# Kernel tuning notes

Hardware: AMD Instinct MI355X
Metric: run time of the kernel (lower is better)

## Reference

```python
import jax, jax.numpy as jnp
import numpy as np
from jax.ops import segment_sum

N = 100000   # nodes
E = 1600000  # edges
D = 128      # node_feature_dim == hidden_dim
DE = 16      # edge_feature_dim
G = 512      # num_graphs
EPS = 1e-5   # BatchNorm eps


def setup_inputs() -> dict:
    key = jax.random.key(0)
    ks = jax.random.split(key, 24)
    inp = {
        "x": jax.random.normal(ks[0], (N, D), jnp.float32),
        "edge_index": jax.random.randint(ks[1], (2, E), 0, N, jnp.int64),
        "batch_idx": jnp.sort(jax.random.randint(ks[2], (N,), 0, G, jnp.int64)),
        "edge_attr": jax.random.normal(ks[3], (E, DE), jnp.float32),
        "num_graphs": G,
    }
    s = 1.0 / np.sqrt(D)
    # GCN layer 1 (D -> D) + BatchNorm1d (eval-mode running stats)
    inp["W1"] = jax.random.normal(ks[4], (D, D), jnp.float32) * s
    inp["b1"] = jnp.zeros((D,), jnp.float32)
    inp["g1"] = jax.random.uniform(ks[5], (D,), jnp.float32, 0.5, 1.5)
    inp["bt1"] = jax.random.normal(ks[6], (D,), jnp.float32) * 0.1
    inp["m1"] = jax.random.normal(ks[7], (D,), jnp.float32) * 0.1
    inp["v1"] = jax.random.uniform(ks[8], (D,), jnp.float32, 0.5, 1.5)
    # GCN layer 2
    inp["W2"] = jax.random.normal(ks[9], (D, D), jnp.float32) * s
    inp["b2"] = jnp.zeros((D,), jnp.float32)
    inp["g2"] = jax.random.uniform(ks[10], (D,), jnp.float32, 0.5, 1.5)
    inp["bt2"] = jax.random.normal(ks[11], (D,), jnp.float32) * 0.1
    inp["m2"] = jax.random.normal(ks[12], (D,), jnp.float32) * 0.1
    inp["v2"] = jax.random.uniform(ks[13], (D,), jnp.float32, 0.5, 1.5)
    # edge encoder: Linear(DE,D) -> ReLU -> Linear(D,D)
    inp["We1"] = jax.random.normal(ks[14], (DE, D), jnp.float32) / np.sqrt(DE)
    inp["be1"] = jnp.zeros((D,), jnp.float32)
    inp["We2"] = jax.random.normal(ks[15], (D, D), jnp.float32) * s
    inp["be2"] = jnp.zeros((D,), jnp.float32)
    return inp


def _gcn_conv(x, W, b, src, dst, n):
    # PyG GCNConv: add self-loops, sym norm D^-1/2 (A+I) D^-1/2, then X W + b
    xw = x @ W  # [n, out]
    loops = jnp.arange(n, dtype=src.dtype)
    s = jnp.concatenate([src, loops])
    d = jnp.concatenate([dst, loops])
    deg = segment_sum(jnp.ones_like(d, dtype=xw.dtype), d, num_segments=n)
    dinv = jnp.where(deg > 0, jax.lax.rsqrt(jnp.maximum(deg, 1.0)), 0.0)
    norm = dinv[s] * dinv[d]  # [e+n]
    msg = xw[s] * norm[:, None]
    return segment_sum(msg, d, num_segments=n) + b


def _bn_relu(x, g, bt, m, v):
    return jax.nn.relu((x - m) * jax.lax.rsqrt(v + EPS) * g + bt)


def reference(x, edge_index, batch_idx, edge_attr, num_graphs,
              W1, b1, g1, bt1, m1, v1,
              W2, b2, g2, bt2, m2, v2,
              We1, be1, We2, be2):
    n = x.shape[0]
    src, dst = edge_index[0], edge_index[1]
    # two GraphConvLayer: GCNConv -> BN(eval) -> ReLU -> Dropout(eval=id)
    h = _bn_relu(_gcn_conv(x, W1, b1, src, dst, n), g1, bt1, m1, v1)
    h = _bn_relu(_gcn_conv(h, W2, b2, src, dst, n), g2, bt2, m2, v2)
    # global mean pool over nodes per graph
    nsum = segment_sum(h, batch_idx, num_segments=num_graphs)
    ncnt = segment_sum(jnp.ones((n,), h.dtype), batch_idx, num_segments=num_graphs)
    graph_repr = nsum / jnp.maximum(ncnt, 1.0)[:, None]
    # edge encoder + per-graph edge mean (fused segment-mean)
    e = jax.nn.relu(edge_attr @ We1 + be1) @ We2 + be2  # [E, D]
    edge_batch = batch_idx[src]
    esum = segment_sum(e, edge_batch, num_segments=num_graphs)
    ecnt = segment_sum(jnp.ones((e.shape[0],), e.dtype), edge_batch, num_segments=num_graphs)
    edge_repr = jnp.where(ecnt[:, None] > 0, esum / jnp.maximum(ecnt, 1.0)[:, None], 0.0)
    return graph_repr + edge_repr
```

## Files before the change

kernel.cpp:

```cpp
#include <hip/hip_runtime.h>

#define N_NODES 100000
#define N_EDGES 1600000
#define D 128
#define DE 16
#define G 512
#define EPSBN 1e-5f
#define ESLICE 4
#define EPB 1024
#define EPT (EPB / 256)
#define SCHUNK 1024
#define NSB ((N_NODES + SCHUNK - 1) / SCHUNK)
#define AGG_CH 16
#define DSHIFT 9
#define DBSZ 512
#define NBKT ((N_NODES + DBSZ - 1) / DBSZ)

typedef __bf16 bf16x8 __attribute__((ext_vector_type(8)));
typedef __bf16 bf16x4 __attribute__((ext_vector_type(4)));
typedef float f32x4 __attribute__((ext_vector_type(4)));

__device__ __forceinline__ float bf_lo(unsigned v) { return __uint_as_float(v << 16); }
__device__ __forceinline__ float bf_hi(unsigned v) { return __uint_as_float(v & 0xffff0000u); }

__global__ void k_init(int* __restrict__ deg, int* __restrict__ ecnt, int* __restrict__ dcnt,
                       float* __restrict__ gcnt, float* __restrict__ gsum,
                       float* __restrict__ esum) {
  int i = blockIdx.x * 256 + threadIdx.x;
  if (i < N_NODES) deg[i] = 1;
  if (i < G) { ecnt[i] = 0; gcnt[i] = 0.f; }
  if (i < NBKT) dcnt[i] = 0;
  if (i < G * D) { gsum[i] = 0.f; esum[i] = 0.f; }
}

__global__ void k_count(const int* __restrict__ ei, const int* __restrict__ batch,
                        int* __restrict__ deg, int* __restrict__ ecnt, int* __restrict__ dcnt) {
  __shared__ int bins[G];
  __shared__ int dbins[NBKT];
  int tid = threadIdx.x;
  for (int i = tid; i < G; i += 256) bins[i] = 0;
  for (int i = tid; i < NBKT; i += 256) dbins[i] = 0;
  __syncthreads();
  int base = blockIdx.x * 4096;
  for (int t = tid; t < 4096; t += 256) {
    int e = base + t;
    if (e < N_EDGES) {
      int s = ei[e];
      int d = ei[N_EDGES + e];
      atomicAdd(&deg[d], 1);
      atomicAdd(&bins[batch[s]], 1);
      atomicAdd(&dbins[d >> DSHIFT], 1);
    }
  }
  __syncthreads();
  for (int i = tid; i < G; i += 256) if (bins[i]) atomicAdd(&ecnt[i], bins[i]);
  for (int i = tid; i < NBKT; i += 256) if (dbins[i]) atomicAdd(&dcnt[i], dbins[i]);
}

__global__ __launch_bounds__(256) void k_scan_part(const int* __restrict__ deg,
                                                   int* __restrict__ part) {
  __shared__ int red[4];
  int tid = threadIdx.x;
  int base = blockIdx.x * SCHUNK + tid * 4;
  int s = 0;
  #pragma unroll
  for (int k = 0; k < 4; ++k) {
    int i = base + k;
    if (i < N_NODES) s += deg[i];
  }
  #pragma unroll
  for (int off = 32; off > 0; off >>= 1) s += __shfl_down(s, off);
  if ((tid & 63) == 0) red[tid >> 6] = s;
  __syncthreads();
  if (tid == 0) part[blockIdx.x] = red[0] + red[1] + red[2] + red[3];
}

__global__ void k_scan_mid(int* __restrict__ part, const int* __restrict__ ecnt,
                           int* __restrict__ ebs, int* __restrict__ ecur_pad,
                           const int* __restrict__ dcnt, int* __restrict__ dbs,
                           int* __restrict__ dcur_pad) {
  __shared__ int sb[512];
  int tid = threadIdx.x;
  int v = (tid < NSB) ? part[tid] : 0;
  sb[tid] = v;
  __syncthreads();
  for (int off = 1; off < 512; off <<= 1) {
    int t = (tid >= off) ? sb[tid - off] : 0;
    __syncthreads();
    sb[tid] += t;
    __syncthreads();
  }
  if (tid < NSB) part[tid] = sb[tid] - v;
  __syncthreads();
  int v2 = ecnt[tid];
  sb[tid] = v2;
  __syncthreads();
  for (int off = 1; off < 512; off <<= 1) {
    int t = (tid >= off) ? sb[tid - off] : 0;
    __syncthreads();
    sb[tid] += t;
    __syncthreads();
  }
  ebs[tid] = sb[tid] - v2;
  ecur_pad[tid * 16] = sb[tid] - v2;
  __syncthreads();
  int v3 = (tid < NBKT) ? dcnt[tid] : 0;
  sb[tid] = v3;
  __syncthreads();
  for (int off = 1; off < 512; off <<= 1) {
    int t = (tid >= off) ? sb[tid - off] : 0;
    __syncthreads();
    sb[tid] += t;
    __syncthreads();
  }
  if (tid < NBKT) { dbs[tid] = sb[tid] - v3; dcur_pad[tid * 16] = sb[tid] - v3; }
}

__global__ __launch_bounds__(256) void k_scan_write(const int* __restrict__ deg,
                                                    const int* __restrict__ part,
                                                    int* __restrict__ rs,
                                                    float* __restrict__ dinv) {
  __shared__ int sb[256];
  int tid = threadIdx.x;
  int base = blockIdx.x * SCHUNK + tid * 4;
  int d[4];
  int s = 0;
  #pragma unroll
  for (int k = 0; k < 4; ++k) {
    int i = base + k;
    d[k] = (i < N_NODES) ? deg[i] : 0;
    s += d[k];
  }
  sb[tid] = s;
  __syncthreads();
  for (int off = 1; off < 256; off <<= 1) {
    int t = (tid >= off) ? sb[tid - off] : 0;
    __syncthreads();
    sb[tid] += t;
    __syncthreads();
  }
  int ex = sb[tid] - s + part[blockIdx.x];
  #pragma unroll
  for (int k = 0; k < 4; ++k) {
    int i = base + k;
    if (i < N_NODES) {
      rs[i] = ex;
      dinv[i] = rsqrtf((float)d[k]);
      ex += d[k];
    }
  }
}

__global__ __launch_bounds__(256) void k_scatter(const int* __restrict__ ei,
                                                 const int* __restrict__ batch,
                                                 const float* __restrict__ edge_attr,
                                                 int* __restrict__ ecur_pad,
                                                 int* __restrict__ dcur_pad,
                                                 int2* __restrict__ pairs,
                                                 __bf16* __restrict__ eaS) {
  __shared__ int gbins[G];
  __shared__ int gbase[G];
  __shared__ int dbins[NBKT];
  __shared__ int dbase[NBKT];
  int tid = threadIdx.x;
  for (int i = tid; i < G; i += 256) gbins[i] = 0;
  for (int i = tid; i < NBKT; i += 256) dbins[i] = 0;
  __syncthreads();
  int e0 = blockIdx.x * EPB;
  int ge[EPT], gr[EPT], db[EPT], dr[EPT];
  #pragma unroll
  for (int k = 0; k < EPT; ++k) {
    int e = e0 + k * 256 + tid;
    ge[k] = -1;
    if (e < N_EDGES) {
      int s = ei[e], d = ei[N_EDGES + e];
      int g = batch[s];
      ge[k] = g;
      gr[k] = atomicAdd(&gbins[g], 1);
      db[k] = d >> DSHIFT;
      dr[k] = atomicAdd(&dbins[db[k]], 1);
    }
  }
  __syncthreads();
  for (int i = tid; i < G; i += 256) {
    int cnt = gbins[i];
    gbase[i] = cnt ? atomicAdd(&ecur_pad[i * 16], cnt) : 0;
  }
  for (int i = tid; i < NBKT; i += 256) {
    int cnt = dbins[i];
    dbase[i] = cnt ? atomicAdd(&dcur_pad[i * 16], cnt) : 0;
  }
  __syncthreads();
  #pragma unroll
  for (int k = 0; k < EPT; ++k) {
    if (ge[k] >= 0) {
      int e = e0 + k * 256 + tid;
      int s = ei[e], d = ei[N_EDGES + e];
      int gpos = gbase[ge[k]] + gr[k];
      const float4* p = (const float4*)(edge_attr + (size_t)e * DE);
      float4 f0 = p[0], f1 = p[1], f2 = p[2], f3 = p[3];
      bf16x8 h0, h1;
      h0[0] = (__bf16)f0.x; h0[1] = (__bf16)f0.y; h0[2] = (__bf16)f0.z; h0[3] = (__bf16)f0.w;
      h0[4] = (__bf16)f1.x; h0[5] = (__bf16)f1.y; h0[6] = (__bf16)f1.z; h0[7] = (__bf16)f1.w;
      h1[0] = (__bf16)f2.x; h1[1] = (__bf16)f2.y; h1[2] = (__bf16)f2.z; h1[3] = (__bf16)f2.w;
      h1[4] = (__bf16)f3.x; h1[5] = (__bf16)f3.y; h1[6] = (__bf16)f3.z; h1[7] = (__bf16)f3.w;
      bf16x8* q = (bf16x8*)(eaS + (size_t)gpos * DE);
      q[0] = h0; q[1] = h1;
      pairs[dbase[db[k]] + dr[k]] = make_int2(s, d);
    }
  }
}

__global__ __launch_bounds__(256) void k_scatter_nbr(const int2* __restrict__ pairs,
                                                     const int* __restrict__ dbs,
                                                     const int* __restrict__ dcnt,
                                                     const int* __restrict__ rs,
                                                     int* __restrict__ nbr) {
  __shared__ int cur[DBSZ];
  int tid = threadIdx.x;
  int bkt = blockIdx.x;
  int nodeBase = bkt << DSHIFT;
  for (int l = tid; l < DBSZ; l += 256) {
    int node = nodeBase + l;
    cur[l] = (node < N_NODES) ? rs[node] : 0;
  }
  __syncthreads();
  int start = dbs[bkt], n = dcnt[bkt];
  for (int i = tid; i < n; i += 256) {
    int2 p = pairs[start + i];
    int pos = atomicAdd(&cur[p.y - nodeBase], 1);
    nbr[pos] = p.x;
  }
}

__global__ void k_prep_w(const float* __restrict__ W, __bf16* __restrict__ Wf) {
  int tid = threadIdx.x;
  for (int idx = blockIdx.x * 256 + tid; idx < 16384; idx += 8 * 256) {
    int j = idx & 7;
    int lane = (idx >> 3) & 63;
    int cb = (idx >> 9) & 7;
    int kc = idx >> 12;
    int k = kc * 32 + (lane >> 4) * 8 + j;
    int n = cb * 16 + (lane & 15);
    Wf[idx] = (__bf16)W[k * 128 + n];
  }
}

__global__ __launch_bounds__(256) void k_gemm_mfma(const float* __restrict__ X,
                                                   const __bf16* __restrict__ Wf,
                                                   const float* __restrict__ dinv,
                                                   __bf16* __restrict__ out) {
  __shared__ __bf16 sXb[64][136];
  int tid = threadIdx.x;
  int wave = tid >> 6, lane = tid & 63;
  int m = lane & 15, kg = lane >> 4;
  int base = blockIdx.x * 64;
  #pragma unroll
  for (int i = 0; i < 8; ++i) {
    int idx = tid + i * 256;
    int r = idx >> 5, cq = idx & 31;
    int row = base + r;
    float4 v = make_float4(0.f, 0.f, 0.f, 0.f);
    if (row < N_NODES) v = *(const float4*)(X + (size_t)row * 128 + cq * 4);
    bf16x4 h;
    h[0] = (__bf16)v.x; h[1] = (__bf16)v.y; h[2] = (__bf16)v.z; h[3] = (__bf16)v.w;
    *(bf16x4*)(&sXb[r][cq * 4]) = h;
  }
  __syncthreads();
  int r0 = wave * 16;
  f32x4 acc[8];
  #pragma unroll
  for (int cb = 0; cb < 8; ++cb) acc[cb] = (f32x4){0.f, 0.f, 0.f, 0.f};
  #pragma unroll
  for (int kc = 0; kc < 4; ++kc) {
    bf16x8 afrag = *(const bf16x8*)(&sXb[r0 + m][kc * 32 + kg * 8]);
    #pragma unroll
    for (int cb = 0; cb < 8; ++cb) {
      bf16x8 bfrag = *(const bf16x8*)(Wf + (((size_t)(kc * 8 + cb) * 64 + lane) << 3));
      acc[cb] = __builtin_amdgcn_mfma_f32_16x16x32_bf16(afrag, bfrag, acc[cb], 0, 0, 0);
    }
  }
  #pragma unroll
  for (int r = 0; r < 4; ++r) {
    int grow = base + r0 + kg * 4 + r;
    if (grow < N_NODES) {
      float dv = dinv[grow];
      #pragma unroll
      for (int cb = 0; cb < 8; ++cb)
        out[(size_t)grow * 128 + cb * 16 + m] = (__bf16)(acc[cb][r] * dv);
    }
  }
}

__global__ __launch_bounds__(256) void k_agg_bn(const unsigned* __restrict__ Au,
                                                const int* __restrict__ nbr,
                                                const int* __restrict__ rs,
                                                const int* __restrict__ deg,
                                                const float* __restrict__ dinv,
                                                const float* __restrict__ b,
                                                const float* __restrict__ gm,
                                                const float* __restrict__ bt,
                                                const float* __restrict__ m,
                                                const float* __restrict__ v,
                                                float* __restrict__ outB) {
  int tid = threadIdx.x;
  int wave = tid >> 6, lane = tid & 63;
  int c0 = lane * 2, c1 = c0 + 1;
  float sc0 = gm[c0] * rsqrtf(v[c0] + EPSBN), sc1 = gm[c1] * rsqrtf(v[c1] + EPSBN);
  float sh0 = bt[c0] - m[c0] * sc0, sh1 = bt[c1] - m[c1] * sc1;
  float bb0 = b[c0], bb1 = b[c1];
  int base = (blockIdx.x * 4 + wave) * AGG_CH;
  for (int nn = 0; nn < AGG_CH; ++nn) {
    int i = base + nn;
    if (i >= N_NODES) return;
    unsigned sv = Au[(size_t)i * 64 + lane];
    float s0 = bf_lo(sv), s1 = bf_hi(sv);
    int j = rs[i];
    int end = j + deg[i] - 1;
    for (; j + 3 < end; j += 4) {
      int n0 = nbr[j], n1 = nbr[j + 1], n2 = nbr[j + 2], n3 = nbr[j + 3];
      unsigned a0 = Au[(size_t)n0 * 64 + lane];
      unsigned a1 = Au[(size_t)n1 * 64 + lane];
      unsigned a2 = Au[(size_t)n2 * 64 + lane];
      unsigned a3 = Au[(size_t)n3 * 64 + lane];
      s0 += bf_lo(a0) + bf_lo(a1) + bf_lo(a2) + bf_lo(a3);
      s1 += bf_hi(a0) + bf_hi(a1) + bf_hi(a2) + bf_hi(a3);
    }
    for (; j < end; ++j) {
      unsigned a = Au[(size_t)nbr[j] * 64 + lane];
      s0 += bf_lo(a); s1 += bf_hi(a);
    }
    float dv = dinv[i];
    float y0 = fmaxf((dv * s0 + bb0) * sc0 + sh0, 0.f);
    float y1 = fmaxf((dv * s1 + bb1) * sc1 + sh1, 0.f);
    *(float2*)(outB + (size_t)i * 128 + c0) = make_float2(y0, y1);
  }
}

__global__ __launch_bounds__(256) void k_agg_bn_pool(const unsigned* __restrict__ Au,
                                                     const int* __restrict__ nbr,
                                                     const int* __restrict__ rs,
                                                     const int* __restrict__ deg,
                                                     const float* __restrict__ dinv,
                                                     const int* __restrict__ batch,
                                                     const float* __restrict__ b,
                                                     const float* __restrict__ gm,
                                                     const float* __restrict__ bt,
                                                     const float* __restrict__ m,
                                                     const float* __restrict__ v,
                                                     float* __restrict__ gsum,
                                                     float* __restrict__ gcnt) {
  int tid = threadIdx.x;
  int wave = tid >> 6, lane = tid & 63;
  int c0 = lane * 2, c1 = c0 + 1;
  float sc0 = gm[c0] * rsqrtf(v[c0] + EPSBN), sc1 = gm[c1] * rsqrtf(v[c1] + EPSBN);
  float sh0 = bt[c0] - m[c0] * sc0, sh1 = bt[c1] - m[c1] * sc1;
  float bb0 = b[c0], bb1 = b[c1];
  int base = (blockIdx.x * 4 + wave) * AGG_CH;
  if (base >= N_NODES) return;
  float acc0 = 0.f, acc1 = 0.f, cnt = 0.f;
  int curg = -1;
  for (int nn = 0; nn < AGG_CH; ++nn) {
    int i = base + nn;
    if (i >= N_NODES) break;
    int bg = batch[i];
    if (bg != curg) {
      if (curg >= 0) {
        atomicAdd(&gsum[(size_t)curg * 128 + c0], acc0);
        atomicAdd(&gsum[(size_t)curg * 128 + c1], acc1);
        if (lane == 0) atomicAdd(&gcnt[curg], cnt);
      }
      acc0 = 0.f; acc1 = 0.f; cnt = 0.f; curg = bg;
    }
    unsigned sv = Au[(size_t)i * 64 + lane];
    float s0 = bf_lo(sv), s1 = bf_hi(sv);
    int j = rs[i];
    int end = j + deg[i] - 1;
    for (; j + 3 < end; j += 4) {
      int n0 = nbr[j], n1 = nbr[j + 1], n2 = nbr[j + 2], n3 = nbr[j + 3];
      unsigned a0 = Au[(size_t)n0 * 64 + lane];
      unsigned a1 = Au[(size_t)n1 * 64 + lane];
      unsigned a2 = Au[(size_t)n2 * 64 + lane];
      unsigned a3 = Au[(size_t)n3 * 64 + lane];
      s0 += bf_lo(a0) + bf_lo(a1) + bf_lo(a2) + bf_lo(a3);
      s1 += bf_hi(a0) + bf_hi(a1) + bf_hi(a2) + bf_hi(a3);
    }
    for (; j < end; ++j) {
      unsigned a = Au[(size_t)nbr[j] * 64 + lane];
      s0 += bf_lo(a); s1 += bf_hi(a);
    }
    float dv = dinv[i];
    acc0 += fmaxf((dv * s0 + bb0) * sc0 + sh0, 0.f);
    acc1 += fmaxf((dv * s1 + bb1) * sc1 + sh1, 0.f);
    cnt += 1.f;
  }
  if (curg >= 0) {
    atomicAdd(&gsum[(size_t)curg * 128 + c0], acc0);
    atomicAdd(&gsum[(size_t)curg * 128 + c1], acc1);
    if (lane == 0) atomicAdd(&gcnt[curg], cnt);
  }
}

__global__ __launch_bounds__(256) void k_edge_hidden(
    const __bf16* __restrict__ eaS,
    const int* __restrict__ ebs, const int* __restrict__ ecnt,
    const float* __restrict__ We1, const float* __restrict__ be1,
    float* __restrict__ esum) {
  int tid = threadIdx.x;
  int wave = tid >> 6;
  int lane = tid & 63;
  int n = lane & 15;
  int kg = lane >> 4;
  int g = blockIdx.x / ESLICE;
  int slice = blockIdx.x % ESLICE;

  bf16x8 bfrag[8];
  float biasv[8];
  #pragma unroll
  for (int blk = 0; blk < 8; ++blk) {
    #pragma unroll
    for (int j = 0; j < 8; ++j) {
      int k = kg * 8 + j;
      float w = (k < DE) ? We1[k * 128 + blk * 16 + n] : 0.f;
      bfrag[blk][j] = (__bf16)w;
    }
    biasv[blk] = be1[blk * 16 + n];
  }

  int start = ebs[g], cnt = ecnt[g];
  int lim = start + cnt;
  int ntiles = (cnt + 15) >> 4;
  const int nstream = ESLICE * 4;
  int sid = slice * 4 + wave;
  int tpc = (ntiles + nstream - 1) / nstream;
  int t0 = sid * tpc;
  int t1 = t0 + tpc; if (t1 > ntiles) t1 = ntiles;

  float racc[8] = {0.f, 0.f, 0.f, 0.f, 0.f, 0.f, 0.f, 0.f};

  for (int t = t0; t < t1; ++t) {
    int jb = start + (t << 4);
    int row = jb + n;
    int rc = row < lim - 1 ? row : lim - 1;
    bf16x8 afrag = {};
    if (kg < 2) afrag = *(const bf16x8*)(eaS + (size_t)rc * DE + kg * 8);
    bool full = (jb + 16 <= lim);
    if (full) {
      #pragma unroll
      for (int blk = 0; blk < 8; ++blk) {
        f32x4 acc = {0.f, 0.f, 0.f, 0.f};
        acc = __builtin_amdgcn_mfma_f32_16x16x32_bf16(afrag, bfrag[blk], acc, 0, 0, 0);
        #pragma unroll
        for (int r = 0; r < 4; ++r)
          racc[blk] += fmaxf(acc[r] + biasv[blk], 0.f);
      }
    } else {
      #pragma unroll
      for (int blk = 0; blk < 8; ++blk) {
        f32x4 acc = {0.f, 0.f, 0.f, 0.f};
        acc = __builtin_amdgcn_mfma_f32_16x16x32_bf16(afrag, bfrag[blk], acc, 0, 0, 0);
        #pragma unroll
        for (int r = 0; r < 4; ++r) {
          int rr = kg * 4 + r;
          if (jb + rr < lim) racc[blk] += fmaxf(acc[r] + biasv[blk], 0.f);
        }
      }
    }
  }

  #pragma unroll
  for (int blk = 0; blk < 8; ++blk) {
    float vsum = racc[blk];
    vsum += __shfl_xor(vsum, 16);
    vsum += __shfl_xor(vsum, 32);
    if (lane < 16) atomicAdd(&esum[(size_t)g * 128 + blk * 16 + n], vsum);
  }
}

__global__ void k_final(const float* __restrict__ esum, const int* __restrict__ ecnt,
                        const float* __restrict__ gsum, const float* __restrict__ gcnt,
                        const float* __restrict__ We2, const float* __restrict__ be2,
                        float* __restrict__ out) {
  __shared__ float mh[128];
  int g = blockIdx.x, c = threadIdx.x;
  int ec = ecnt[g];
  mh[c] = (ec > 0) ? esum[(size_t)g * 128 + c] / (float)ec : 0.f;
  __syncthreads();
  float acc = 0.f;
  #pragma unroll 8
  for (int k = 0; k < 128; ++k) acc += mh[k] * We2[k * 128 + c];
  float er = (ec > 0) ? (acc + be2[c]) : 0.f;
  float gr = gsum[(size_t)g * 128 + c] / fmaxf(gcnt[g], 1.f);
  out[(size_t)g * 128 + c] = gr + er;
}

extern "C" void kernel_launch(void* const* d_in, const int* in_sizes, int n_in,
                              void* d_out, int out_size, void* d_ws, size_t ws_size,
                              hipStream_t stream) {
  const float* x        = (const float*)d_in[0];
  const int*   ei       = (const int*)d_in[1];
  const int*   batch    = (const int*)d_in[2];
  const float* edge_attr= (const float*)d_in[3];
  const float* W1 = (const float*)d_in[5];
  const float* b1 = (const float*)d_in[6];
  const float* g1 = (const float*)d_in[7];
  const float* bt1= (const float*)d_in[8];
  const float* m1 = (const float*)d_in[9];
  const float* v1 = (const float*)d_in[10];
  const float* W2 = (const float*)d_in[11];
  const float* b2 = (const float*)d_in[12];
  const float* g2 = (const float*)d_in[13];
  const float* bt2= (const float*)d_in[14];
  const float* m2 = (const float*)d_in[15];
  const float* v2 = (const float*)d_in[16];
  const float* We1= (const float*)d_in[17];
  const float* be1= (const float*)d_in[18];
  const float* We2= (const float*)d_in[19];
  const float* be2= (const float*)d_in[20];
  float* out = (float*)d_out;

  char* ws = (char*)d_ws;
  size_t off = 0;
  auto take = [&](size_t bytes) -> char* {
    char* p = ws + off;
    off += (bytes + 255) & ~(size_t)255;
    return p;
  };
  __bf16* A       = (__bf16*)take((size_t)N_NODES * 128 * 2);
  float*  B       = (float*) take((size_t)N_NODES * 128 * 4);
  float*  dinv    = (float*) take((size_t)N_NODES * 4);
  int*    deg     = (int*)   take((size_t)N_NODES * 4);
  int*    rs      = (int*)   take((size_t)N_NODES * 4);
  int*    nbr     = (int*)   take((size_t)(N_EDGES + N_NODES) * 4);
  int2*   pairs   = (int2*)  take((size_t)N_EDGES * 8);
  __bf16* eaS     = (__bf16*)take((size_t)N_EDGES * DE * 2);
  __bf16* Wf1     = (__bf16*)take((size_t)16384 * 2);
  __bf16* Wf2     = (__bf16*)take((size_t)16384 * 2);
  int*    ecnt    = (int*)   take((size_t)G * 4);
  int*    ebs     = (int*)   take((size_t)G * 4);
  int*    ecur_pad= (int*)   take((size_t)G * 16 * 4);
  int*    dcnt    = (int*)   take((size_t)NBKT * 4);
  int*    dbs     = (int*)   take((size_t)NBKT * 4);
  int*    dcur_pad= (int*)   take((size_t)NBKT * 16 * 4);
  float*  gcnt    = (float*) take((size_t)G * 4);
  float*  esum    = (float*) take((size_t)G * 128 * 4);
  float*  gsum    = (float*) take((size_t)G * 128 * 4);
  int*    part    = (int*)   take((size_t)NSB * 4);

  k_init<<<(N_NODES + 255) / 256, 256, 0, stream>>>(deg, ecnt, dcnt, gcnt, gsum, esum);
  k_prep_w<<<8, 256, 0, stream>>>(W1, Wf1);
  k_prep_w<<<8, 256, 0, stream>>>(W2, Wf2);
  k_count<<<(N_EDGES + 4095) / 4096, 256, 0, stream>>>(ei, batch, deg, ecnt, dcnt);
  k_scan_part<<<NSB, 256, 0, stream>>>(deg, part);
  k_scan_mid<<<1, 512, 0, stream>>>(part, ecnt, ebs, ecur_pad, dcnt, dbs, dcur_pad);
  k_scan_write<<<NSB, 256, 0, stream>>>(deg, part, rs, dinv);
  k_scatter<<<(N_EDGES + EPB - 1) / EPB, 256, 0, stream>>>(ei, batch, edge_attr, ecur_pad, dcur_pad, pairs, eaS);
  k_scatter_nbr<<<NBKT, 256, 0, stream>>>(pairs, dbs, dcnt, rs, nbr);
  const int aggBlocks = (N_NODES + 4 * AGG_CH - 1) / (4 * AGG_CH);
  k_gemm_mfma<<<(N_NODES + 63) / 64, 256, 0, stream>>>(x, Wf1, dinv, A);
  k_agg_bn<<<aggBlocks, 256, 0, stream>>>((const unsigned*)A, nbr, rs, deg, dinv, b1, g1, bt1, m1, v1, B);
  k_gemm_mfma<<<(N_NODES + 63) / 64, 256, 0, stream>>>(B, Wf2, dinv, A);
  k_agg_bn_pool<<<aggBlocks, 256, 0, stream>>>((const unsigned*)A, nbr, rs, deg, dinv, batch, b2, g2, bt2, m2, v2, gsum, gcnt);
  k_edge_hidden<<<G * ESLICE, 256, 0, stream>>>(eaS, ebs, ecnt, We1, be1, esum);
  k_final<<<G, 128, 0, stream>>>(esum, ecnt, gsum, gcnt, We2, be2, out);
}
```

Baseline: 727.9 us.

## Sort edges locally in shared memory before scattering to coalesce writes

The edge-bucketing scatter kernel now takes 2048 edges per block. It prefix-scans the per-graph and per-destination-bucket histograms in shared memory and builds local permutations, so consecutive threads write to consecutive output slots. The aim is to turn the scattered bf16 edge-attribute stores and the (src,dst) pair stores into mostly contiguous runs within each bucket. The cost is extra shared memory (four 2048-int arrays), several barrier-heavy scan rounds, and gathered reads of edge_attr and edge_index in permuted order. The scan assumes 256 threads and exactly 512 graph bins, and NBKT must stay at or below 256.

```diff
diff --git a/kernel.cpp b/kernel.cpp
--- a/kernel.cpp
+++ b/kernel.cpp
@@ -7,7 +7,7 @@
 #define G 512
 #define EPSBN 1e-5f
 #define ESLICE 4
-#define EPB 1024
+#define EPB 2048
 #define EPT (EPB / 256)
 #define SCHUNK 1024
 #define NSB ((N_NODES + SCHUNK - 1) / SCHUNK)
@@ -162,11 +162,17 @@
   __shared__ int gbase[G];
   __shared__ int dbins[NBKT];
   __shared__ int dbase[NBKT];
+  __shared__ int gsrc[EPB];
+  __shared__ int gdst[EPB];
+  __shared__ int dsrc[EPB];
+  __shared__ int ddst[EPB];
   int tid = threadIdx.x;
   for (int i = tid; i < G; i += 256) gbins[i] = 0;
   for (int i = tid; i < NBKT; i += 256) dbins[i] = 0;
   __syncthreads();
   int e0 = blockIdx.x * EPB;
+  int nvalid = N_EDGES - e0;
+  if (nvalid > EPB) nvalid = EPB;
   int ge[EPT], gr[EPT], db[EPT], dr[EPT];
   #pragma unroll
   for (int k = 0; k < EPT; ++k) {
@@ -190,24 +196,56 @@
     int cnt = dbins[i];
     dbase[i] = cnt ? atomicAdd(&dcur_pad[i * 16], cnt) : 0;
   }
+  int v0 = gbins[tid], v1 = gbins[tid + 256];
+  int vd = (tid < NBKT) ? dbins[tid] : 0;
+  gsrc[tid] = vd;
+  __syncthreads();
+  for (int off = 1; off < 512; off <<= 1) {
+    int a = (tid >= off) ? gbins[tid - off] : 0;
+    int b = gbins[tid + 256 - off];
+    int c = (off < 256 && tid >= off) ? gsrc[tid - off] : 0;
+    __syncthreads();
+    gbins[tid] += a;
+    gbins[tid + 256] += b;
+    if (off < 256) gsrc[tid] += c;
+    __syncthreads();
+  }
+  gbins[tid] -= v0;
+  gbins[tid + 256] -= v1;
+  if (tid < NBKT) dbins[tid] = gsrc[tid] - vd;
   __syncthreads();
   #pragma unroll
   for (int k = 0; k < EPT; ++k) {
     if (ge[k] >= 0) {
       int e = e0 + k * 256 + tid;
-      int s = ei[e], d = ei[N_EDGES + e];
-      int gpos = gbase[ge[k]] + gr[k];
-      const float4* p = (const float4*)(edge_attr + (size_t)e * DE);
-      float4 f0 = p[0], f1 = p[1], f2 = p[2], f3 = p[3];
-      bf16x8 h0, h1;
-      h0[0] = (__bf16)f0.x; h0[1] = (__bf16)f0.y; h0[2] = (__bf16)f0.z; h0[3] = (__bf16)f0.w;
-      h0[4] = (__bf16)f1.x; h0[5] = (__bf16)f1.y; h0[6] = (__bf16)f1.z; h0[7] = (__bf16)f1.w;
-      h1[0] = (__bf16)f2.x; h1[1] = (__bf16)f2.y; h1[2] = (__bf16)f2.z; h1[3] = (__bf16)f2.w;
-      h1[4] = (__bf16)f3.x; h1[5] = (__bf16)f3.y; h1[6] = (__bf16)f3.z; h1[7] = (__bf16)f3.w;
-      bf16x8* q = (bf16x8*)(eaS + (size_t)gpos * DE);
-      q[0] = h0; q[1] = h1;
-      pairs[dbase[db[k]] + dr[k]] = make_int2(s, d);
-    }
+      int g = ge[k];
+      int sG = gbins[g] + gr[k];
+      gsrc[sG] = e;
+      gdst[sG] = gbase[g] + gr[k];
+      int bkt = db[k];
+      int sD = dbins[bkt] + dr[k];
+      dsrc[sD] = e;
+      ddst[sD] = dbase[bkt] + dr[k];
+    }
+  }
+  __syncthreads();
+  for (int p = tid; p < nvalid; p += 256) {
+    int e = gsrc[p];
+    int dst = gdst[p];
+    const float4* q = (const float4*)(edge_attr + (size_t)e * DE);
+    float4 f0 = q[0], f1 = q[1], f2 = q[2], f3 = q[3];
+    bf16x8 h0, h1;
+    h0[0] = (__bf16)f0.x; h0[1] = (__bf16)f0.y; h0[2] = (__bf16)f0.z; h0[3] = (__bf16)f0.w;
+    h0[4] = (__bf16)f1.x; h0[5] = (__bf16)f1.y; h0[6] = (__bf16)f1.z; h0[7] = (__bf16)f1.w;
+    h1[0] = (__bf16)f2.x; h1[1] = (__bf16)f2.y; h1[2] = (__bf16)f2.z; h1[3] = (__bf16)f2.w;
+    h1[4] = (__bf16)f3.x; h1[5] = (__bf16)f3.y; h1[6] = (__bf16)f3.z; h1[7] = (__bf16)f3.w;
+    bf16x8* w = (bf16x8*)(eaS + (size_t)dst * DE);
+    w[0] = h0; w[1] = h1;
+  }
+  for (int p = tid; p < nvalid; p += 256) {
+    int e = dsrc[p];
+    int s = ei[e], d = ei[N_EDGES + e];
+    pairs[ddst[p]] = make_int2(s, d);
   }
 }
 
```

Measured after the change: 716.8 us. No clear change (-1.5%).
